# Performance work log

Hardware: AMD Instinct MI355X
Metric: run time of the kernel (lower is better)

The kernel has to match this reference:

```python
import jax, jax.numpy as jnp
import numpy as np

EMBED = 2048
HEADS = 32
HEAD_DIM = EMBED // HEADS
Q_BITS = 4
Q_MAX = 2 ** (Q_BITS - 1) - 1  # 7
DECOMP = 8
CHUNK = 256


def _sym_qdq(x, scale):
    # sym_quant followed by sym_dequant (float32 math, clamp to [-8, 7])
    s = jnp.clip(jnp.abs(scale), 1e-9, None)
    return jnp.clip(jnp.round(x / s), -(Q_MAX + 1), Q_MAX) * s


def _quant_weight(w):
    # per-output-channel symmetric int4 quant-dequant of weight [out, in]
    w = w.astype(jnp.float32)
    s = jnp.max(jnp.abs(w), axis=-1, keepdims=True) / Q_MAX
    return _sym_qdq(w, s)


def _chunk_decompose(x2d):
    """Tender chunked activation quantization.
    Splits rows into chunks of CHUNK, subtracts per-chunk channel bias,
    groups channels into DECOMP scale groups by their column max, and
    applies per-group int4 quant-dequant. Vectorized over the DECOMP groups
    (the masks partition channels, so a per-channel scale gather is exact).
    """
    T, H = x2d.shape
    chunks = (T + CHUNK - 1) // CHUNK
    pad = chunks * CHUNK - T
    xp = jnp.pad(x2d, ((0, pad), (0, 0))).reshape(chunks, CHUNK, H).astype(jnp.float32)
    ch_bias = (jnp.max(xp, axis=1, keepdims=True) + jnp.min(xp, axis=1, keepdims=True)) / 2
    xz = xp - ch_bias                                   # [chunks, CHUNK, H]
    tmax = jnp.max(jnp.abs(xz), axis=(1, 2))            # [chunks]
    cmax = jnp.max(jnp.abs(xz), axis=1)                 # [chunks, H]
    # thresholds t_i = tmax / 2^(DECOMP-1-i), ascending in i
    thr = tmax[:, None] / (2.0 ** jnp.arange(DECOMP - 1, -1, -1, dtype=jnp.float32))
    # group index: i=0 if cmax<=t0, else first i with t_{i-1} < cmax <= t_i
    idx = jnp.sum(cmax[:, :, None] > thr[:, None, : DECOMP - 1], axis=-1)  # [chunks, H]
    scale = tmax[:, None] / (2.0 ** (DECOMP - 1 - idx).astype(jnp.float32)) / Q_MAX
    result = _sym_qdq(xz, scale[:, None, :])            # [chunks, CHUNK, H]
    return result, ch_bias, T


def reference(hidden_states, q_weight, k_weight, v_weight, o_weight,
              q_bias, k_bias, v_bias, o_bias):
    bsz, tgt, H = hidden_states.shape
    # int4 dequantized weights, transposed for right-multiply
    WQ = _quant_weight(q_weight).T
    WK = _quant_weight(k_weight).T
    WV = _quant_weight(v_weight).T
    WO = _quant_weight(o_weight).T

    result, ch_bias, n = _chunk_decompose(hidden_states.reshape(bsz * tgt, H))

    def proj(w_orig, w_dq_t, b):
        # bias-corrected dequant GEMM: per-chunk channel bias uses the
        # ORIGINAL (fp) weight, quantized residual uses the int4 weight
        y = result @ w_dq_t + ch_bias @ w_orig.astype(jnp.float32).T
        return y.reshape(-1, H)[:n] + b

    scaling = HEAD_DIM ** -0.5
    Q = (proj(q_weight, WQ, q_bias) * scaling).reshape(bsz, tgt, HEADS, HEAD_DIM)
    K = proj(k_weight, WK, k_bias).reshape(bsz, tgt, HEADS, HEAD_DIM)
    V = proj(v_weight, WV, v_bias).reshape(bsz, tgt, HEADS, HEAD_DIM)

    # quant_mha == False path: plain attention
    attn = jnp.einsum('bqhd,bkhd->bhqk', Q, K)
    probs = jax.nn.softmax(attn, axis=-1)
    ctx = jnp.einsum('bhqk,bkhd->bqhd', probs, V).reshape(bsz * tgt, H)

    # output projection through the same chunked quant pipeline
    r2, cb2, n2 = _chunk_decompose(ctx)
    out = (r2 @ WO + cb2 @ o_weight.astype(jnp.float32).T).reshape(-1, H)[:n2] + o_bias
    return out.reshape(bsz, tgt, H)


def setup_inputs() -> dict:
    key = jax.random.key(0)
    ks = jax.random.split(key, 10)
    B, T = 2, 1024
    inp = {
        'hidden_states': jax.random.normal(ks[0], (B, T, EMBED), dtype=jnp.float32),
        'q_weight': jax.random.normal(ks[1], (EMBED, EMBED), dtype=jnp.float32) * 0.02,
        'k_weight': jax.random.normal(ks[2], (EMBED, EMBED), dtype=jnp.float32) * 0.02,
        'v_weight': jax.random.normal(ks[3], (EMBED, EMBED), dtype=jnp.float32) * 0.02,
        'o_weight': jax.random.normal(ks[4], (EMBED, EMBED), dtype=jnp.float32) * 0.02,
        'q_bias': jax.random.normal(ks[5], (EMBED,), dtype=jnp.float32) * 0.02,
        'k_bias': jax.random.normal(ks[6], (EMBED,), dtype=jnp.float32) * 0.02,
        'v_bias': jax.random.normal(ks[7], (EMBED,), dtype=jnp.float32) * 0.02,
        'o_bias': jax.random.normal(ks[8], (EMBED,), dtype=jnp.float32) * 0.02,
    }
    return inp
```

## Files before the change

kernel.cpp:

```cpp
#include <hip/hip_runtime.h>
#include <hip/hip_bf16.h>

typedef unsigned short u16;
typedef unsigned int u32;
typedef __attribute__((ext_vector_type(8))) short bs8;
typedef __attribute__((ext_vector_type(4))) float fx4;
typedef __attribute__((ext_vector_type(4))) float f4_t;
typedef __attribute__((ext_vector_type(4))) unsigned int u4_t;

#define HDIM 2048
#define NCH 8

__device__ inline u16 f2bf(float f) {
  __hip_bfloat16 h = __float2bfloat16(f);
  return __builtin_bit_cast(u16, h);
}
__device__ inline float bf2f(u16 u) {
  __hip_bfloat16 h = __builtin_bit_cast(__hip_bfloat16, u);
  return __bfloat162float(h);
}
__device__ inline float pow2i(int e) {
  return __builtin_bit_cast(float, (unsigned)((127 + e) << 23));
}
__device__ inline void gld_lds16(const void* g, void* l) {
  __builtin_amdgcn_global_load_lds((const __attribute__((address_space(1))) void*)g,
                                   (__attribute__((address_space(3))) void*)l, 16, 0, 0);
}

__global__ __launch_bounds__(256) void k_wquant_cbw(
    const float* __restrict__ w0, const float* __restrict__ w1,
    const float* __restrict__ w2, const float* __restrict__ bias,
    u16* __restrict__ wq, float* __restrict__ sw, float* __restrict__ cbw,
    int NC) {
  int o = blockIdx.x, t = threadIdx.x;
  const float* w = (o < 2048) ? w0 : ((o < 4096) ? w1 : w2);
  const float* wrow = w + (size_t)(o & 2047) * HDIM;
  const f4_t* row4 = (const f4_t*)wrow;
  f4_t x0 = row4[2 * t], x1 = row4[2 * t + 1];
  float am = 0.f;
#pragma unroll
  for (int j = 0; j < 4; j++) { am = fmaxf(am, fabsf(x0[j])); am = fmaxf(am, fabsf(x1[j])); }
#pragma unroll
  for (int m = 1; m < 64; m <<= 1) am = fmaxf(am, __shfl_xor(am, m));
  __shared__ float red[4];
  if ((t & 63) == 0) red[t >> 6] = am;
  __syncthreads();
  am = fmaxf(fmaxf(red[0], red[1]), fmaxf(red[2], red[3]));
  float s = fmaxf(am / 7.0f, 1e-9f);
  if (t == 0) sw[o] = s;
  bs8 ov;
#pragma unroll
  for (int j = 0; j < 4; j++) {
    float q0 = fminf(fmaxf(rintf(x0[j] / s), -8.f), 7.f);
    float q1 = fminf(fmaxf(rintf(x1[j] / s), -8.f), 7.f);
    ov[j]     = (short)f2bf(q0);
    ov[j + 4] = (short)f2bf(q1);
  }
  ((bs8*)(wq + (size_t)o * HDIM))[t] = ov;
  float acc[NCH];
#pragma unroll
  for (int c = 0; c < NCH; c++) {
    const f4_t* bc = (const f4_t*)(bias + (size_t)c * HDIM);
    f4_t b0 = bc[2 * t], b1 = bc[2 * t + 1];
    float a = 0.f;
#pragma unroll
    for (int j = 0; j < 4; j++) a += x0[j] * b0[j] + x1[j] * b1[j];
    acc[c] = a;
  }
  __shared__ float redc[NCH][4];
#pragma unroll
  for (int c = 0; c < NCH; c++) {
    float a = acc[c];
#pragma unroll
    for (int m = 1; m < 64; m <<= 1) a += __shfl_xor(a, m);
    if ((t & 63) == 0) redc[c][t >> 6] = a;
  }
  __syncthreads();
  if (t < NCH) cbw[t * NC + o] = redc[t][0] + redc[t][1] + redc[t][2] + redc[t][3];
}

__global__ __launch_bounds__(256) void k_stats(const float* __restrict__ x,
                                               float* __restrict__ biasO,
                                               float* __restrict__ cmaxO) {
  int ch = blockIdx.x >> 3;
  int c = ((blockIdx.x & 7) << 8) + threadIdx.x;
  const float* base = x + (size_t)ch * 256 * HDIM + c;
  float mx = -1e30f, mn = 1e30f;
  for (int r = 0; r < 256; r++) { float v = base[(size_t)r * HDIM]; mx = fmaxf(mx, v); mn = fminf(mn, v); }
  float bi = (mx + mn) * 0.5f;
  biasO[ch * HDIM + c] = bi;
  cmaxO[ch * HDIM + c] = fmaxf(mx - bi, bi - mn);
}

__global__ __launch_bounds__(256) void k_tscale(const float* __restrict__ cmax,
                                                float* __restrict__ scaleO,
                                                float* __restrict__ e2O,
                                                float* __restrict__ tcO) {
  int ch = blockIdx.x, t = threadIdx.x;
  const float* cr = cmax + ch * HDIM;
  float v[8];
  float mx = 0.f;
#pragma unroll
  for (int i = 0; i < 8; i++) { v[i] = cr[i * 256 + t]; mx = fmaxf(mx, v[i]); }
#pragma unroll
  for (int m = 1; m < 64; m <<= 1) mx = fmaxf(mx, __shfl_xor(mx, m));
  __shared__ float red[4];
  __shared__ float tms;
  if ((t & 63) == 0) red[t >> 6] = mx;
  __syncthreads();
  if (t == 0) tms = fmaxf(fmaxf(red[0], red[1]), fmaxf(red[2], red[3]));
  __syncthreads();
  float tmax = tms;
  if (t == 0) tcO[ch] = (tmax / 7.0f) * pow2i(-7);
#pragma unroll
  for (int i = 0; i < 8; i++) {
    int idx = 0;
#pragma unroll
    for (int k = 0; k < 7; k++) idx += (v[i] > tmax * pow2i(k - 7)) ? 1 : 0;
    float s = (tmax * pow2i(idx - 7)) / 7.0f;
    scaleO[ch * HDIM + i * 256 + t] = fmaxf(s, 1e-9f);
    e2O[ch * HDIM + i * 256 + t] = pow2i(idx);
  }
}

__global__ __launch_bounds__(256) void k_qdq(const float* __restrict__ x,
                                             const float* __restrict__ bias,
                                             const float* __restrict__ scale,
                                             const float* __restrict__ e2,
                                             u16* __restrict__ out) {
  int row = blockIdx.x, t = threadIdx.x;
  int ch = row >> 8;
  const f4_t* xr = (const f4_t*)(x + (size_t)row * HDIM);
  const f4_t* br = (const f4_t*)(bias + (size_t)ch * HDIM);
  const f4_t* sr = (const f4_t*)(scale + (size_t)ch * HDIM);
  const f4_t* er = (const f4_t*)(e2 + (size_t)ch * HDIM);
  f4_t x0 = xr[2 * t], x1 = xr[2 * t + 1];
  f4_t b0 = br[2 * t], b1 = br[2 * t + 1];
  f4_t s0 = sr[2 * t], s1 = sr[2 * t + 1];
  f4_t e0 = er[2 * t], e1 = er[2 * t + 1];
  bs8 ov;
#pragma unroll
  for (int j = 0; j < 4; j++) {
    float q0 = fminf(fmaxf(rintf((x0[j] - b0[j]) / s0[j]), -8.f), 7.f);
    ov[j] = (short)f2bf(q0 * e0[j]);
    float q1 = fminf(fmaxf(rintf((x1[j] - b1[j]) / s1[j]), -8.f), 7.f);
    ov[j + 4] = (short)f2bf(q1 * e1[j]);
  }
  ((bs8*)(out + (size_t)row * HDIM))[t] = ov;
}

__global__ __launch_bounds__(256) void k_gemm(
    const u16* __restrict__ A, const u16* __restrict__ B,
    float* __restrict__ o0, float* __restrict__ o1, float* __restrict__ o2,
    const float* __restrict__ cbw, int NC,
    const float* __restrict__ bb0, const float* __restrict__ bb1,
    const float* __restrict__ bb2,
    const float* __restrict__ tc, const float* __restrict__ sw,
    float scl0, float scl1, float scl2, int kt0, int kt1) {
  __shared__ u16 smA[128 * 64];
  __shared__ u16 smB[128 * 64];
  int tid = threadIdx.x;
  int wave = tid >> 6, lane = tid & 63;
  int wr = wave >> 1, wc = wave & 1;
  int row0 = blockIdx.y * 128, col0 = blockIdx.x * 128;
  int mat = col0 >> 11;
  float* out = (mat == 0) ? o0 : ((mat == 1) ? o1 : o2);
  const float* bias = (mat == 0) ? bb0 : ((mat == 1) ? bb1 : bb2);
  float scl = (mat == 0) ? scl0 : ((mat == 1) ? scl1 : scl2);
  int chunk = row0 >> 8;
  fx4 zz = {0.f, 0.f, 0.f, 0.f};
  fx4 acc[4][4];
#pragma unroll
  for (int m = 0; m < 4; m++)
#pragma unroll
    for (int n = 0; n < 4; n++) acc[m][n] = zz;

  int srow = wave * 8 + (lane >> 3);
  int scol = (((lane & 7) ^ (lane >> 3)) << 3);
  const u16* Ab = A + (size_t)row0 * HDIM;
  const u16* Bb = B + (size_t)col0 * HDIM;

  int arow = wr * 64 + (lane & 15);
  int brow = wc * 64 + (lane & 15);
  int xA = (arow & 7) << 4;
  int xB = (brow & 7) << 4;
  int kB0 = (lane >> 4) << 4;

  for (int kt = kt0; kt < kt1; kt++) {
    int kb = kt * 64 + scol;
#pragma unroll
    for (int r = 0; r < 4; r++) {
      gld_lds16(Ab + (size_t)(r * 32 + srow) * HDIM + kb,
                (char*)smA + (r * 32 + wave * 8) * 128);
      gld_lds16(Bb + (size_t)(r * 32 + srow) * HDIM + kb,
                (char*)smB + (r * 32 + wave * 8) * 128);
    }
    __syncthreads();
#pragma unroll
    for (int kk = 0; kk < 2; kk++) {
      bs8 af[4], bfr[4];
#pragma unroll
      for (int m = 0; m < 4; m++)
        af[m] = *(const bs8*)((const char*)smA + (size_t)((arow + m * 16) * 128 +
                                ((kk * 64 + kB0) ^ xA)));
#pragma unroll
      for (int n = 0; n < 4; n++)
        bfr[n] = *(const bs8*)((const char*)smB + (size_t)((brow + n * 16) * 128 +
                                ((kk * 64 + kB0) ^ xB)));
#pragma unroll
      for (int m = 0; m < 4; m++)
#pragma unroll
        for (int n = 0; n < 4; n++)
          acc[m][n] = __builtin_amdgcn_mfma_f32_16x16x32_bf16(af[m], bfr[n], acc[m][n], 0, 0, 0);
    }
    __syncthreads();
  }
  if (o0 == nullptr) {
  }
  float tcv = tc[chunk];
  int colb = col0 + wc * 64 + (lane & 15);
  int rowb = row0 + wr * 64 + ((lane >> 4) << 2);
#pragma unroll
  for (int m = 0; m < 4; m++) {
#pragma unroll
    for (int n = 0; n < 4; n++) {
      int colg = colb + n * 16;
      int colL = colg - (mat << 11);
      float sc = tcv * sw[colg];
      float cb = cbw[chunk * NC + colg] + bias[colL];
#pragma unroll
      for (int j = 0; j < 4; j++) {
        int row = rowb + m * 16 + j;
        out[(size_t)row * HDIM + colL] = (acc[m][n][j] * sc + cb) * scl;
      }
    }
  }
}

__global__ __launch_bounds__(256) void k_gemm_sk(const u16* __restrict__ A,
                                                 const u16* __restrict__ B,
                                                 float* __restrict__ pbuf) {
  __shared__ u16 smA[128 * 64];
  __shared__ u16 smB[128 * 64];
  int tid = threadIdx.x;
  int wave = tid >> 6, lane = tid & 63;
  int wr = wave >> 1, wc = wave & 1;
  int row0 = blockIdx.y * 128, col0 = blockIdx.x * 128;
  int z = blockIdx.z;
  float* out = pbuf + (size_t)z * HDIM * HDIM;
  fx4 zz = {0.f, 0.f, 0.f, 0.f};
  fx4 acc[4][4];
#pragma unroll
  for (int m = 0; m < 4; m++)
#pragma unroll
    for (int n = 0; n < 4; n++) acc[m][n] = zz;

  int srow = wave * 8 + (lane >> 3);
  int scol = (((lane & 7) ^ (lane >> 3)) << 3);
  const u16* Ab = A + (size_t)row0 * HDIM;
  const u16* Bb = B + (size_t)col0 * HDIM;

  int arow = wr * 64 + (lane & 15);
  int brow = wc * 64 + (lane & 15);
  int xA = (arow & 7) << 4;
  int xB = (brow & 7) << 4;
  int kB0 = (lane >> 4) << 4;

  for (int kt = z * 16; kt < z * 16 + 16; kt++) {
    int kb = kt * 64 + scol;
#pragma unroll
    for (int r = 0; r < 4; r++) {
      gld_lds16(Ab + (size_t)(r * 32 + srow) * HDIM + kb,
                (char*)smA + (r * 32 + wave * 8) * 128);
      gld_lds16(Bb + (size_t)(r * 32 + srow) * HDIM + kb,
                (char*)smB + (r * 32 + wave * 8) * 128);
    }
    __syncthreads();
#pragma unroll
    for (int kk = 0; kk < 2; kk++) {
      bs8 af[4], bfr[4];
#pragma unroll
      for (int m = 0; m < 4; m++)
        af[m] = *(const bs8*)((const char*)smA + (size_t)((arow + m * 16) * 128 +
                                ((kk * 64 + kB0) ^ xA)));
#pragma unroll
      for (int n = 0; n < 4; n++)
        bfr[n] = *(const bs8*)((const char*)smB + (size_t)((brow + n * 16) * 128 +
                                ((kk * 64 + kB0) ^ xB)));
#pragma unroll
      for (int m = 0; m < 4; m++)
#pragma unroll
        for (int n = 0; n < 4; n++)
          acc[m][n] = __builtin_amdgcn_mfma_f32_16x16x32_bf16(af[m], bfr[n], acc[m][n], 0, 0, 0);
    }
    __syncthreads();
  }
  int colb = col0 + wc * 64 + (lane & 15);
  int rowb = row0 + wr * 64 + ((lane >> 4) << 2);
#pragma unroll
  for (int m = 0; m < 4; m++)
#pragma unroll
    for (int n = 0; n < 4; n++)
#pragma unroll
      for (int j = 0; j < 4; j++)
        out[(size_t)(rowb + m * 16 + j) * HDIM + colb + n * 16] = acc[m][n][j];
}

__global__ __launch_bounds__(256) void k_fin(const float* __restrict__ p0,
                                             const float* __restrict__ p1,
                                             const float* __restrict__ cbw,
                                             const float* __restrict__ bias,
                                             const float* __restrict__ tc,
                                             const float* __restrict__ sw,
                                             float* __restrict__ out) {
  int row = blockIdx.x, t = threadIdx.x;
  int chunk = row >> 8;
  float tcv = tc[chunk];
  const f4_t* a = (const f4_t*)(p0 + (size_t)row * HDIM);
  const f4_t* b = (const f4_t*)(p1 + (size_t)row * HDIM);
  f4_t* o = (f4_t*)(out + (size_t)row * HDIM);
#pragma unroll
  for (int u = 0; u < 2; u++) {
    f4_t x = a[2 * t + u], y = b[2 * t + u];
    f4_t r;
#pragma unroll
    for (int j = 0; j < 4; j++) {
      int c = (2 * t + u) * 4 + j;
      float sc = tcv * sw[c];
      float cb = cbw[chunk * HDIM + c] + bias[c];
      r[j] = ((x[j] + y[j]) * sc + cb) * 1.0f;
    }
    o[2 * t + u] = r;
  }
}

__global__ __launch_bounds__(256) void k_split(const float* __restrict__ Kf,
                                               const float* __restrict__ Vf,
                                               u16* __restrict__ Khg,
                                               u16* __restrict__ Klg,
                                               u16* __restrict__ Vhg,
                                               u16* __restrict__ Vlg) {
  __shared__ u16 Th[4096], Tl[4096];
  int t = threadIdx.x;
  int ti = blockIdx.x & 15, h = (blockIdx.x >> 4) & 31, b = blockIdx.x >> 9;
  size_t rowStart = (size_t)b * 1024 + ti * 64;
  int colh = h * 64;
  size_t tbase = ((size_t)((b * 32 + h) * 16 + ti)) * 4096;
  int kr = t >> 2, d0 = (t & 3) << 4;
  int xk = (kr & 7) << 3;
  const float* kp = Kf + (rowStart + kr) * HDIM + colh + d0;
  const float* vp = Vf + (rowStart + kr) * HDIM + colh + d0;
  f4_t kv[4], vv[4];
#pragma unroll
  for (int qd = 0; qd < 4; qd++) { kv[qd] = *(const f4_t*)(kp + 4 * qd); vv[qd] = *(const f4_t*)(vp + 4 * qd); }
  bs8 h0, l0, h1, l1;
#pragma unroll
  for (int j = 0; j < 4; j++) {
    float x = kv[0][j]; u16 hh = f2bf(x); h0[j] = (short)hh; l0[j] = (short)f2bf(x - bf2f(hh));
    x = kv[1][j]; hh = f2bf(x); h0[j + 4] = (short)hh; l0[j + 4] = (short)f2bf(x - bf2f(hh));
    x = kv[2][j]; hh = f2bf(x); h1[j] = (short)hh; l1[j] = (short)f2bf(x - bf2f(hh));
    x = kv[3][j]; hh = f2bf(x); h1[j + 4] = (short)hh; l1[j + 4] = (short)f2bf(x - bf2f(hh));
  }
  *(bs8*)(Khg + tbase + kr * 64 + (d0 ^ xk)) = h0;
  *(bs8*)(Klg + tbase + kr * 64 + (d0 ^ xk)) = l0;
  *(bs8*)(Khg + tbase + kr * 64 + ((d0 + 8) ^ xk)) = h1;
  *(bs8*)(Klg + tbase + kr * 64 + ((d0 + 8) ^ xk)) = l1;
#pragma unroll
  for (int qd = 0; qd < 4; qd++)
#pragma unroll
    for (int j = 0; j < 4; j++) {
      int d = d0 + 4 * qd + j;
      float x = vv[qd][j]; u16 hh = f2bf(x);
      int vi = d * 64 + (kr ^ ((d & 7) << 3));
      Th[vi] = hh; Tl[vi] = f2bf(x - bf2f(hh));
    }
  __syncthreads();
  *(bs8*)(Vhg + tbase + t * 16) = *(const bs8*)&Th[t * 16];
  *(bs8*)(Vhg + tbase + t * 16 + 8) = *(const bs8*)&Th[t * 16 + 8];
  *(bs8*)(Vlg + tbase + t * 16) = *(const bs8*)&Tl[t * 16];
  *(bs8*)(Vlg + tbase + t * 16 + 8) = *(const bs8*)&Tl[t * 16 + 8];
}

__global__ __launch_bounds__(256) void k_attn(const float* __restrict__ Q,
                                              const u16* __restrict__ Khg,
                                              const u16* __restrict__ Klg,
                                              const u16* __restrict__ Vhg,
                                              const u16* __restrict__ Vlg,
                                              float* __restrict__ O) {
  __shared__ u16 Kh[64 * 64], Kl[64 * 64];
  __shared__ u16 Vh[64 * 64], Vl[64 * 64];
  int tid = threadIdx.x, wave = tid >> 6, lane = tid & 63;
  int l15 = lane & 15, l4 = lane >> 4;
  int lid = blockIdx.x;
  int xcd = lid & 7, jj = lid >> 3;
  int pair = xcd * 8 + (jj >> 4);
  int qt = jj & 15;
  int h = pair & 31, b = pair >> 5;
  size_t rowStart = (size_t)b * 1024;
  int colh = h * 64;
  int qbase = qt * 64 + wave * 16;
  size_t hbase = (size_t)pair * 16 * 4096;

  bs8 qh[2], ql[2];
#pragma unroll
  for (int kk = 0; kk < 2; kk++) {
    const float* qp = Q + (rowStart + qbase + l15) * HDIM + colh + kk * 32 + (l4 << 3);
    f4_t a0 = *(const f4_t*)qp;
    f4_t a1 = *(const f4_t*)(qp + 4);
#pragma unroll
    for (int j = 0; j < 4; j++) {
      float x = a0[j]; u16 hh = f2bf(x);
      qh[kk][j] = (short)hh; ql[kk][j] = (short)f2bf(x - bf2f(hh));
      x = a1[j]; hh = f2bf(x);
      qh[kk][j + 4] = (short)hh; ql[kk][j + 4] = (short)f2bf(x - bf2f(hh));
    }
  }

  fx4 zz = {0.f, 0.f, 0.f, 0.f};
  fx4 oacc[4];
  float mrun = -1e30f, lrun = 0.f;
#pragma unroll
  for (int n = 0; n < 4; n++) oacc[n] = zz;

  const u16* garr = (wave == 0) ? Khg : (wave == 1) ? Klg : (wave == 2) ? Vhg : Vlg;
  u16* larr = (wave == 0) ? Kh : (wave == 1) ? Kl : (wave == 2) ? Vh : Vl;

  int srcA = l15 + ((lane & 16) << 1);
  int srcB = srcA + 16;
  int hiSel = l4 >> 1;

  for (int ti = 0; ti < 16; ti++) {
    const u16* gsrc = garr + hbase + (size_t)ti * 4096 + lane * 8;
#pragma unroll
    for (int seg = 0; seg < 8; seg++)
      gld_lds16(gsrc + seg * 512, larr + seg * 512);
    __syncthreads();

    fx4 sf[4];
#pragma unroll
    for (int n = 0; n < 4; n++) sf[n] = zz;
    __builtin_amdgcn_s_setprio(1);
#pragma unroll
    for (int kk = 0; kk < 2; kk++) {
      int colr = kk * 32 + (l4 << 3);
#pragma unroll
      for (int n = 0; n < 4; n++) {
        int row = n * 16 + l15;
        int ko = row * 64 + (colr ^ ((row & 7) << 3));
        bs8 bh = *(const bs8*)&Kh[ko];
        bs8 bl = *(const bs8*)&Kl[ko];
        sf[n] = __builtin_amdgcn_mfma_f32_16x16x32_bf16(bl, ql[kk], sf[n], 0, 0, 0);
        sf[n] = __builtin_amdgcn_mfma_f32_16x16x32_bf16(bh, ql[kk], sf[n], 0, 0, 0);
        sf[n] = __builtin_amdgcn_mfma_f32_16x16x32_bf16(bl, qh[kk], sf[n], 0, 0, 0);
        sf[n] = __builtin_amdgcn_mfma_f32_16x16x32_bf16(bh, qh[kk], sf[n], 0, 0, 0);
      }
    }
    __builtin_amdgcn_s_setprio(0);
    float tm = sf[0][0];
#pragma unroll
    for (int n = 0; n < 4; n++)
#pragma unroll
      for (int j = 0; j < 4; j++) tm = fmaxf(tm, sf[n][j]);
    tm = fmaxf(tm, __shfl_xor(tm, 16));
    tm = fmaxf(tm, __shfl_xor(tm, 32));
    float mn = fmaxf(mrun, tm);
    float corr = __expf(mrun - mn);
    mrun = mn;
    float rs = 0.f;
#pragma unroll
    for (int n = 0; n < 4; n++)
#pragma unroll
      for (int j = 0; j < 4; j++) { float p = __expf(sf[n][j] - mn); sf[n][j] = p; rs += p; }
    rs += __shfl_xor(rs, 16);
    rs += __shfl_xor(rs, 32);
    lrun = lrun * corr + rs;
#pragma unroll
    for (int n = 0; n < 4; n++)
#pragma unroll
      for (int j = 0; j < 4; j++) oacc[n][j] *= corr;

    u32 hiw[4][2], low[4][2];
#pragma unroll
    for (int n = 0; n < 4; n++) {
      u16 hh0 = f2bf(sf[n][0]), hh1 = f2bf(sf[n][1]);
      u16 hh2 = f2bf(sf[n][2]), hh3 = f2bf(sf[n][3]);
      u16 ll0 = f2bf(sf[n][0] - bf2f(hh0)), ll1 = f2bf(sf[n][1] - bf2f(hh1));
      u16 ll2 = f2bf(sf[n][2] - bf2f(hh2)), ll3 = f2bf(sf[n][3] - bf2f(hh3));
      hiw[n][0] = (u32)hh0 | ((u32)hh1 << 16);
      hiw[n][1] = (u32)hh2 | ((u32)hh3 << 16);
      low[n][0] = (u32)ll0 | ((u32)ll1 << 16);
      low[n][1] = (u32)ll2 | ((u32)ll3 << 16);
    }
    bs8 ph[2], pl[2];
#pragma unroll
    for (int kkv = 0; kkv < 2; kkv++) {
      u4_t wh, wl;
#pragma unroll
      for (int half = 0; half < 2; half++) {
        int src = half ? srcB : srcA;
#pragma unroll
        for (int pr = 0; pr < 2; pr++) {
          int a0 = __shfl((int)hiw[2 * kkv][pr], src);
          int a1 = __shfl((int)hiw[2 * kkv + 1][pr], src);
          wh[half * 2 + pr] = (u32)(hiSel ? a1 : a0);
          int b0 = __shfl((int)low[2 * kkv][pr], src);
          int b1 = __shfl((int)low[2 * kkv + 1][pr], src);
          wl[half * 2 + pr] = (u32)(hiSel ? b1 : b0);
        }
      }
      ph[kkv] = __builtin_bit_cast(bs8, wh);
      pl[kkv] = __builtin_bit_cast(bs8, wl);
    }

    __builtin_amdgcn_s_setprio(1);
#pragma unroll
    for (int kkv = 0; kkv < 2; kkv++) {
      int colr = kkv * 32 + (l4 << 3);
#pragma unroll
      for (int n = 0; n < 4; n++) {
        int vrow = n * 16 + l15;
        int vo = vrow * 64 + (colr ^ ((vrow & 7) << 3));
        bs8 vh = *(const bs8*)&Vh[vo];
        bs8 vl = *(const bs8*)&Vl[vo];
        oacc[n] = __builtin_amdgcn_mfma_f32_16x16x32_bf16(vl, pl[kkv], oacc[n], 0, 0, 0);
        oacc[n] = __builtin_amdgcn_mfma_f32_16x16x32_bf16(vh, pl[kkv], oacc[n], 0, 0, 0);
        oacc[n] = __builtin_amdgcn_mfma_f32_16x16x32_bf16(vl, ph[kkv], oacc[n], 0, 0, 0);
        oacc[n] = __builtin_amdgcn_mfma_f32_16x16x32_bf16(vh, ph[kkv], oacc[n], 0, 0, 0);
      }
    }
    __builtin_amdgcn_s_setprio(0);
    __syncthreads();
  }
  size_t token = rowStart + qbase + l15;
#pragma unroll
  for (int n = 0; n < 4; n++) {
    f4_t r;
#pragma unroll
    for (int j = 0; j < 4; j++) r[j] = oacc[n][j] / lrun;
    *(f4_t*)(O + token * HDIM + colh + n * 16 + (l4 << 2)) = r;
  }
}

extern "C" void kernel_launch(void* const* d_in, const int* in_sizes, int n_in,
                              void* d_out, int out_size, void* d_ws, size_t ws_size,
                              hipStream_t stream) {
  const float* hs = (const float*)d_in[0];
  const float* qw = (const float*)d_in[1];
  const float* kw = (const float*)d_in[2];
  const float* vw = (const float*)d_in[3];
  const float* ow = (const float*)d_in[4];
  const float* qb = (const float*)d_in[5];
  const float* kb = (const float*)d_in[6];
  const float* vb = (const float*)d_in[7];
  const float* ob = (const float*)d_in[8];

  char* ws = (char*)d_ws;
  const size_t MB = 1u << 20;
  u16* wqQKV = (u16*)(ws + 0 * MB);
  u16* actA  = (u16*)(ws + 24 * MB);
  u16* Khg   = (u16*)(ws + 0 * MB);
  u16* Klg   = (u16*)(ws + 8 * MB);
  u16* Vhg   = (u16*)(ws + 16 * MB);
  u16* Vlg   = (u16*)(ws + 24 * MB);
  float* p01 = (float*)(ws + 0 * MB);
  float* Qf  = (float*)(ws + 32 * MB);
  float* Kf  = (float*)(ws + 48 * MB);
  float* Vf  = (float*)(ws + 64 * MB);
  u16* actA2 = (u16*)(ws + 48 * MB);
  u16* wqO   = (u16*)(ws + 64 * MB);
  float* sm  = (float*)(ws + 80 * MB);
  float* bias1  = sm;
  float* cmax1  = bias1 + NCH * HDIM;
  float* scale1 = cmax1 + NCH * HDIM;
  float* e2_1   = scale1 + NCH * HDIM;
  float* bias2  = e2_1 + NCH * HDIM;
  float* cmax2  = bias2 + NCH * HDIM;
  float* scale2 = cmax2 + NCH * HDIM;
  float* e2_2   = scale2 + NCH * HDIM;
  float* cbwQKV = e2_2 + NCH * HDIM;
  float* swQKV  = cbwQKV + NCH * 3 * HDIM;
  float* cbwO   = swQKV + 3 * HDIM;
  float* swO    = cbwO + NCH * HDIM;
  float* tc1    = swO + HDIM;
  float* tc2    = tc1 + NCH;
  float* ctx = (float*)d_out;

  k_stats<<<64, 256, 0, stream>>>(hs, bias1, cmax1);
  k_tscale<<<8, 256, 0, stream>>>(cmax1, scale1, e2_1, tc1);
  k_qdq<<<2048, 256, 0, stream>>>(hs, bias1, scale1, e2_1, actA);
  k_wquant_cbw<<<6144, 256, 0, stream>>>(qw, kw, vw, bias1, wqQKV, swQKV, cbwQKV, 3 * HDIM);
  k_gemm<<<dim3(48, 16), 256, 0, stream>>>(actA, wqQKV, Qf, Kf, Vf,
                                           cbwQKV, 3 * HDIM, qb, kb, vb,
                                           tc1, swQKV, 0.125f, 1.0f, 1.0f, 0, 32);
  k_split<<<1024, 256, 0, stream>>>(Kf, Vf, Khg, Klg, Vhg, Vlg);
  k_attn<<<1024, 256, 0, stream>>>(Qf, Khg, Klg, Vhg, Vlg, ctx);
  k_stats<<<64, 256, 0, stream>>>(ctx, bias2, cmax2);
  k_tscale<<<8, 256, 0, stream>>>(cmax2, scale2, e2_2, tc2);
  k_qdq<<<2048, 256, 0, stream>>>(ctx, bias2, scale2, e2_2, actA2);
  k_wquant_cbw<<<2048, 256, 0, stream>>>(ow, ow, ow, bias2, wqO, swO, cbwO, HDIM);
  k_gemm_sk<<<dim3(16, 16, 2), 256, 0, stream>>>(actA2, wqO, p01);
  k_fin<<<2048, 256, 0, stream>>>(p01, p01 + (size_t)HDIM * HDIM,
                                  cbwO, ob, tc2, swO, (float*)d_out);
}
```

Measured before the change: 281.2 us.

## Replace split-K output GEMM plus finalize kernel with fused 64x128-tile GEMM

```diff
diff --git a/kernel.cpp b/kernel.cpp
--- a/kernel.cpp
+++ b/kernel.cpp
@@ -215,8 +215,6 @@
     }
     __syncthreads();
   }
-  if (o0 == nullptr) {
-  }
   float tcv = tc[chunk];
   int colb = col0 + wc * 64 + (lane & 15);
   int rowb = row0 + wr * 64 + ((lane >> 4) << 2);
@@ -237,21 +235,22 @@
   }
 }
 
-__global__ __launch_bounds__(256) void k_gemm_sk(const u16* __restrict__ A,
-                                                 const u16* __restrict__ B,
-                                                 float* __restrict__ pbuf) {
-  __shared__ u16 smA[128 * 64];
+__global__ __launch_bounds__(256) void k_gemm_o(
+    const u16* __restrict__ A, const u16* __restrict__ B,
+    float* __restrict__ out, const float* __restrict__ cbw,
+    const float* __restrict__ bias, const float* __restrict__ tc,
+    const float* __restrict__ sw) {
+  __shared__ u16 smA[64 * 64];
   __shared__ u16 smB[128 * 64];
   int tid = threadIdx.x;
   int wave = tid >> 6, lane = tid & 63;
   int wr = wave >> 1, wc = wave & 1;
-  int row0 = blockIdx.y * 128, col0 = blockIdx.x * 128;
-  int z = blockIdx.z;
-  float* out = pbuf + (size_t)z * HDIM * HDIM;
+  int row0 = blockIdx.y * 64, col0 = blockIdx.x * 128;
+  int chunk = row0 >> 8;
   fx4 zz = {0.f, 0.f, 0.f, 0.f};
-  fx4 acc[4][4];
-#pragma unroll
-  for (int m = 0; m < 4; m++)
+  fx4 acc[2][4];
+#pragma unroll
+  for (int m = 0; m < 2; m++)
 #pragma unroll
     for (int n = 0; n < 4; n++) acc[m][n] = zz;
 
@@ -260,27 +259,28 @@
   const u16* Ab = A + (size_t)row0 * HDIM;
   const u16* Bb = B + (size_t)col0 * HDIM;
 
-  int arow = wr * 64 + (lane & 15);
+  int arow = wr * 32 + (lane & 15);
   int brow = wc * 64 + (lane & 15);
   int xA = (arow & 7) << 4;
   int xB = (brow & 7) << 4;
   int kB0 = (lane >> 4) << 4;
 
-  for (int kt = z * 16; kt < z * 16 + 16; kt++) {
+  for (int kt = 0; kt < 32; kt++) {
     int kb = kt * 64 + scol;
 #pragma unroll
-    for (int r = 0; r < 4; r++) {
+    for (int r = 0; r < 2; r++)
       gld_lds16(Ab + (size_t)(r * 32 + srow) * HDIM + kb,
                 (char*)smA + (r * 32 + wave * 8) * 128);
+#pragma unroll
+    for (int r = 0; r < 4; r++)
       gld_lds16(Bb + (size_t)(r * 32 + srow) * HDIM + kb,
                 (char*)smB + (r * 32 + wave * 8) * 128);
-    }
     __syncthreads();
 #pragma unroll
     for (int kk = 0; kk < 2; kk++) {
-      bs8 af[4], bfr[4];
-#pragma unroll
-      for (int m = 0; m < 4; m++)
+      bs8 af[2], bfr[4];
+#pragma unroll
+      for (int m = 0; m < 2; m++)
         af[m] = *(const bs8*)((const char*)smA + (size_t)((arow + m * 16) * 128 +
                                 ((kk * 64 + kB0) ^ xA)));
 #pragma unroll
@@ -288,49 +288,29 @@
         bfr[n] = *(const bs8*)((const char*)smB + (size_t)((brow + n * 16) * 128 +
                                 ((kk * 64 + kB0) ^ xB)));
 #pragma unroll
-      for (int m = 0; m < 4; m++)
+      for (int m = 0; m < 2; m++)
 #pragma unroll
         for (int n = 0; n < 4; n++)
           acc[m][n] = __builtin_amdgcn_mfma_f32_16x16x32_bf16(af[m], bfr[n], acc[m][n], 0, 0, 0);
     }
     __syncthreads();
   }
+  float tcv = tc[chunk];
   int colb = col0 + wc * 64 + (lane & 15);
-  int rowb = row0 + wr * 64 + ((lane >> 4) << 2);
-#pragma unroll
-  for (int m = 0; m < 4; m++)
-#pragma unroll
-    for (int n = 0; n < 4; n++)
-#pragma unroll
-      for (int j = 0; j < 4; j++)
-        out[(size_t)(rowb + m * 16 + j) * HDIM + colb + n * 16] = acc[m][n][j];
-}
-
-__global__ __launch_bounds__(256) void k_fin(const float* __restrict__ p0,
-                                             const float* __restrict__ p1,
-                                             const float* __restrict__ cbw,
-                                             const float* __restrict__ bias,
-                                             const float* __restrict__ tc,
-                                             const float* __restrict__ sw,
-                                             float* __restrict__ out) {
-  int row = blockIdx.x, t = threadIdx.x;
-  int chunk = row >> 8;
-  float tcv = tc[chunk];
-  const f4_t* a = (const f4_t*)(p0 + (size_t)row * HDIM);
-  const f4_t* b = (const f4_t*)(p1 + (size_t)row * HDIM);
-  f4_t* o = (f4_t*)(out + (size_t)row * HDIM);
-#pragma unroll
-  for (int u = 0; u < 2; u++) {
-    f4_t x = a[2 * t + u], y = b[2 * t + u];
-    f4_t r;
-#pragma unroll
-    for (int j = 0; j < 4; j++) {
-      int c = (2 * t + u) * 4 + j;
-      float sc = tcv * sw[c];
-      float cb = cbw[chunk * HDIM + c] + bias[c];
-      r[j] = ((x[j] + y[j]) * sc + cb) * 1.0f;
-    }
-    o[2 * t + u] = r;
+  int rowb = row0 + wr * 32 + ((lane >> 4) << 2);
+#pragma unroll
+  for (int m = 0; m < 2; m++) {
+#pragma unroll
+    for (int n = 0; n < 4; n++) {
+      int col = colb + n * 16;
+      float sc = tcv * sw[col];
+      float cb = cbw[chunk * HDIM + col] + bias[col];
+#pragma unroll
+      for (int j = 0; j < 4; j++) {
+        int row = rowb + m * 16 + j;
+        out[(size_t)row * HDIM + col] = (acc[m][n][j] * sc + cb) * 1.0f;
+      }
+    }
   }
 }
 
@@ -562,7 +542,6 @@
   u16* Klg   = (u16*)(ws + 8 * MB);
   u16* Vhg   = (u16*)(ws + 16 * MB);
   u16* Vlg   = (u16*)(ws + 24 * MB);
-  float* p01 = (float*)(ws + 0 * MB);
   float* Qf  = (float*)(ws + 32 * MB);
   float* Kf  = (float*)(ws + 48 * MB);
   float* Vf  = (float*)(ws + 64 * MB);
@@ -598,7 +577,5 @@
   k_tscale<<<8, 256, 0, stream>>>(cmax2, scale2, e2_2, tc2);
   k_qdq<<<2048, 256, 0, stream>>>(ctx, bias2, scale2, e2_2, actA2);
   k_wquant_cbw<<<2048, 256, 0, stream>>>(ow, ow, ow, bias2, wqO, swO, cbwO, HDIM);
-  k_gemm_sk<<<dim3(16, 16, 2), 256, 0, stream>>>(actA2, wqO, p01);
-  k_fin<<<2048, 256, 0, stream>>>(p01, p01 + (size_t)HDIM * HDIM,
-                                  cbwO, ob, tc2, swO, (float*)d_out);
-}
+  k_gemm_o<<<dim3(16, 32), 256, 0, stream>>>(actA2, wqO, (float*)d_out, cbwO, ob, tc2, swO);
+}
```

Measured after the change: 274.6 us. -2.3%, faster.

## Split column stats into partial+combine passes and halve split-K GEMM row tile

Applied to the files above, without the earlier changes.

```diff
diff --git a/kernel.cpp b/kernel.cpp
--- a/kernel.cpp
+++ b/kernel.cpp
@@ -79,14 +79,32 @@
   if (t < NCH) cbw[t * NC + o] = redc[t][0] + redc[t][1] + redc[t][2] + redc[t][3];
 }
 
-__global__ __launch_bounds__(256) void k_stats(const float* __restrict__ x,
-                                               float* __restrict__ biasO,
-                                               float* __restrict__ cmaxO) {
+__global__ __launch_bounds__(256) void k_stats_p(const float* __restrict__ x,
+                                                 float* __restrict__ pmx,
+                                                 float* __restrict__ pmn) {
+  int rg = blockIdx.x & 7;
+  int sl = (blockIdx.x >> 3) & 7;
+  int ch = blockIdx.x >> 6;
+  int c = (sl << 8) + threadIdx.x;
+  const float* base = x + ((size_t)ch * 256 + rg * 32) * HDIM + c;
+  float mx = -1e30f, mn = 1e30f;
+  for (int r = 0; r < 32; r++) { float v = base[(size_t)r * HDIM]; mx = fmaxf(mx, v); mn = fminf(mn, v); }
+  pmx[(size_t)(rg * 8 + ch) * HDIM + c] = mx;
+  pmn[(size_t)(rg * 8 + ch) * HDIM + c] = mn;
+}
+
+__global__ __launch_bounds__(256) void k_stats_c(const float* __restrict__ pmx,
+                                                 const float* __restrict__ pmn,
+                                                 float* __restrict__ biasO,
+                                                 float* __restrict__ cmaxO) {
   int ch = blockIdx.x >> 3;
   int c = ((blockIdx.x & 7) << 8) + threadIdx.x;
-  const float* base = x + (size_t)ch * 256 * HDIM + c;
   float mx = -1e30f, mn = 1e30f;
-  for (int r = 0; r < 256; r++) { float v = base[(size_t)r * HDIM]; mx = fmaxf(mx, v); mn = fminf(mn, v); }
+#pragma unroll
+  for (int rg = 0; rg < 8; rg++) {
+    mx = fmaxf(mx, pmx[(size_t)(rg * 8 + ch) * HDIM + c]);
+    mn = fminf(mn, pmn[(size_t)(rg * 8 + ch) * HDIM + c]);
+  }
   float bi = (mx + mn) * 0.5f;
   biasO[ch * HDIM + c] = bi;
   cmaxO[ch * HDIM + c] = fmaxf(mx - bi, bi - mn);
@@ -215,8 +233,6 @@
     }
     __syncthreads();
   }
-  if (o0 == nullptr) {
-  }
   float tcv = tc[chunk];
   int colb = col0 + wc * 64 + (lane & 15);
   int rowb = row0 + wr * 64 + ((lane >> 4) << 2);
@@ -240,18 +256,18 @@
 __global__ __launch_bounds__(256) void k_gemm_sk(const u16* __restrict__ A,
                                                  const u16* __restrict__ B,
                                                  float* __restrict__ pbuf) {
-  __shared__ u16 smA[128 * 64];
+  __shared__ u16 smA[64 * 64];
   __shared__ u16 smB[128 * 64];
   int tid = threadIdx.x;
   int wave = tid >> 6, lane = tid & 63;
   int wr = wave >> 1, wc = wave & 1;
-  int row0 = blockIdx.y * 128, col0 = blockIdx.x * 128;
+  int row0 = blockIdx.y * 64, col0 = blockIdx.x * 128;
   int z = blockIdx.z;
   float* out = pbuf + (size_t)z * HDIM * HDIM;
   fx4 zz = {0.f, 0.f, 0.f, 0.f};
-  fx4 acc[4][4];
-#pragma unroll
-  for (int m = 0; m < 4; m++)
+  fx4 acc[2][4];
+#pragma unroll
+  for (int m = 0; m < 2; m++)
 #pragma unroll
     for (int n = 0; n < 4; n++) acc[m][n] = zz;
 
@@ -260,7 +276,7 @@
   const u16* Ab = A + (size_t)row0 * HDIM;
   const u16* Bb = B + (size_t)col0 * HDIM;
 
-  int arow = wr * 64 + (lane & 15);
+  int arow = wr * 32 + (lane & 15);
   int brow = wc * 64 + (lane & 15);
   int xA = (arow & 7) << 4;
   int xB = (brow & 7) << 4;
@@ -269,18 +285,19 @@
   for (int kt = z * 16; kt < z * 16 + 16; kt++) {
     int kb = kt * 64 + scol;
 #pragma unroll
-    for (int r = 0; r < 4; r++) {
+    for (int r = 0; r < 2; r++)
       gld_lds16(Ab + (size_t)(r * 32 + srow) * HDIM + kb,
                 (char*)smA + (r * 32 + wave * 8) * 128);
+#pragma unroll
+    for (int r = 0; r < 4; r++)
       gld_lds16(Bb + (size_t)(r * 32 + srow) * HDIM + kb,
                 (char*)smB + (r * 32 + wave * 8) * 128);
-    }
     __syncthreads();
 #pragma unroll
     for (int kk = 0; kk < 2; kk++) {
-      bs8 af[4], bfr[4];
-#pragma unroll
-      for (int m = 0; m < 4; m++)
+      bs8 af[2], bfr[4];
+#pragma unroll
+      for (int m = 0; m < 2; m++)
         af[m] = *(const bs8*)((const char*)smA + (size_t)((arow + m * 16) * 128 +
                                 ((kk * 64 + kB0) ^ xA)));
 #pragma unroll
@@ -288,7 +305,7 @@
         bfr[n] = *(const bs8*)((const char*)smB + (size_t)((brow + n * 16) * 128 +
                                 ((kk * 64 + kB0) ^ xB)));
 #pragma unroll
-      for (int m = 0; m < 4; m++)
+      for (int m = 0; m < 2; m++)
 #pragma unroll
         for (int n = 0; n < 4; n++)
           acc[m][n] = __builtin_amdgcn_mfma_f32_16x16x32_bf16(af[m], bfr[n], acc[m][n], 0, 0, 0);
@@ -296,9 +313,9 @@
     __syncthreads();
   }
   int colb = col0 + wc * 64 + (lane & 15);
-  int rowb = row0 + wr * 64 + ((lane >> 4) << 2);
-#pragma unroll
-  for (int m = 0; m < 4; m++)
+  int rowb = row0 + wr * 32 + ((lane >> 4) << 2);
+#pragma unroll
+  for (int m = 0; m < 2; m++)
 #pragma unroll
     for (int n = 0; n < 4; n++)
 #pragma unroll
@@ -562,12 +579,17 @@
   u16* Klg   = (u16*)(ws + 8 * MB);
   u16* Vhg   = (u16*)(ws + 16 * MB);
   u16* Vlg   = (u16*)(ws + 24 * MB);
-  float* p01 = (float*)(ws + 0 * MB);
+  float* p0  = (float*)(ws + 0 * MB);
+  float* p1  = (float*)(ws + 16 * MB);
   float* Qf  = (float*)(ws + 32 * MB);
   float* Kf  = (float*)(ws + 48 * MB);
   float* Vf  = (float*)(ws + 64 * MB);
   u16* actA2 = (u16*)(ws + 48 * MB);
   u16* wqO   = (u16*)(ws + 64 * MB);
+  float* pmx1 = (float*)(ws + 48 * MB);
+  float* pmn1 = pmx1 + 64 * HDIM;
+  float* pmx2 = (float*)(ws + 32 * MB);
+  float* pmn2 = pmx2 + 64 * HDIM;
   float* sm  = (float*)(ws + 80 * MB);
   float* bias1  = sm;
   float* cmax1  = bias1 + NCH * HDIM;
@@ -585,7 +607,8 @@
   float* tc2    = tc1 + NCH;
   float* ctx = (float*)d_out;
 
-  k_stats<<<64, 256, 0, stream>>>(hs, bias1, cmax1);
+  k_stats_p<<<512, 256, 0, stream>>>(hs, pmx1, pmn1);
+  k_stats_c<<<64, 256, 0, stream>>>(pmx1, pmn1, bias1, cmax1);
   k_tscale<<<8, 256, 0, stream>>>(cmax1, scale1, e2_1, tc1);
   k_qdq<<<2048, 256, 0, stream>>>(hs, bias1, scale1, e2_1, actA);
   k_wquant_cbw<<<6144, 256, 0, stream>>>(qw, kw, vw, bias1, wqQKV, swQKV, cbwQKV, 3 * HDIM);
@@ -594,11 +617,11 @@
                                            tc1, swQKV, 0.125f, 1.0f, 1.0f, 0, 32);
   k_split<<<1024, 256, 0, stream>>>(Kf, Vf, Khg, Klg, Vhg, Vlg);
   k_attn<<<1024, 256, 0, stream>>>(Qf, Khg, Klg, Vhg, Vlg, ctx);
-  k_stats<<<64, 256, 0, stream>>>(ctx, bias2, cmax2);
+  k_stats_p<<<512, 256, 0, stream>>>(ctx, pmx2, pmn2);
+  k_stats_c<<<64, 256, 0, stream>>>(pmx2, pmn2, bias2, cmax2);
   k_tscale<<<8, 256, 0, stream>>>(cmax2, scale2, e2_2, tc2);
   k_qdq<<<2048, 256, 0, stream>>>(ctx, bias2, scale2, e2_2, actA2);
   k_wquant_cbw<<<2048, 256, 0, stream>>>(ow, ow, ow, bias2, wqO, swO, cbwO, HDIM);
-  k_gemm_sk<<<dim3(16, 16, 2), 256, 0, stream>>>(actA2, wqO, p01);
-  k_fin<<<2048, 256, 0, stream>>>(p01, p01 + (size_t)HDIM * HDIM,
-                                  cbwO, ob, tc2, swO, (float*)d_out);
-}
+  k_gemm_sk<<<dim3(16, 32, 2), 256, 0, stream>>>(actA2, wqO, p0);
+  k_fin<<<2048, 256, 0, stream>>>(p0, p1, cbwO, ob, tc2, swO, (float*)d_out);
+}
```

After: 267.2 us. 5.0% less time.
